# Optimization experiments

Measured on AMD Instinct MI355X. Metric: run time of the kernel, lower is better.

## Reference

```python
import jax, jax.numpy as jnp
from jax import lax
import numpy as np

LRELU = 0.01

def conv(x, w, b=None, stride=1, pad=0):
    y = lax.conv_general_dilated(x, w, (stride, stride), [(pad, pad), (pad, pad)],
                                 dimension_numbers=('NCHW', 'OIHW', 'NCHW'))
    return y if b is None else y + b[None, :, None, None]

def deconv(x, w, b, stride=2, pad=1):
    # torch ConvTranspose2d (w: [Cin, Cout, k, k]) == lhs-dilated conv with flipped kernel
    k = w.shape[2]
    wf = jnp.transpose(jnp.flip(w, (2, 3)), (1, 0, 2, 3))  # -> OIHW
    y = lax.conv_general_dilated(x, wf, (1, 1), [(k - 1 - pad, k - 1 - pad)] * 2,
                                 lhs_dilation=(stride, stride),
                                 dimension_numbers=('NCHW', 'OIHW', 'NCHW'))
    return y + b[None, :, None, None]

def bn(x, g, b, eps=1e-5):
    # training-mode BatchNorm2d: batch statistics over (N, H, W)
    m = x.mean((0, 2, 3), keepdims=True)
    v = x.var((0, 2, 3), keepdims=True)
    return (x - m) * lax.rsqrt(v + eps) * g[None, :, None, None] + b[None, :, None, None]

def resblock(x, w1, g1, b1, w2, g2, b2):
    h = jax.nn.relu(bn(conv(x, w1, pad=1), g1, b1))
    return x + bn(conv(h, w2), g2, b2)

def vq_quantize(z, emb, beta=0.25):
    zt = jnp.transpose(z, (0, 2, 3, 1))              # [B,H,W,D]
    D = zt.shape[-1]
    flat = zt.reshape(-1, D)                         # [M,D]
    dist = ((flat ** 2).sum(1, keepdims=True) + (emb ** 2).sum(1)
            - 2.0 * flat @ emb.T)                    # [M,K]
    idx = jnp.argmin(dist, axis=1)                   # [M]
    q = emb[idx].reshape(zt.shape)                   # gather == one-hot @ emb
    loss = beta * jnp.mean((lax.stop_gradient(q) - zt) ** 2)
    q_st = zt + lax.stop_gradient(q - zt)            # straight-through estimator
    counts = jnp.zeros((emb.shape[0],), flat.dtype).at[idx].add(1.0)
    probs = counts / flat.shape[0]
    perplexity = jnp.exp(-jnp.sum(probs * jnp.log(probs + 1e-10)))
    return jnp.transpose(q_st, (0, 3, 1, 2)), loss, perplexity

def vqvae_forward(p, x):
    h = jax.nn.leaky_relu(conv(x, p['e1w'], p['e1b'], 2, 1), LRELU)
    h = jax.nn.leaky_relu(conv(h, p['e2w'], p['e2b'], 2, 1), LRELU)
    h = jax.nn.leaky_relu(conv(h, p['e3w'], p['e3b'], 1, 1), LRELU)
    h = resblock(h, p['er1w'], p['er1g'], p['er1b'], p['er2w'], p['er2g'], p['er2b'])
    h = jax.nn.leaky_relu(h, LRELU)
    encoded = jax.nn.leaky_relu(conv(h, p['e4w'], p['e4b']), LRELU)
    quantized, vq_loss, _ = vq_quantize(encoded, p['emb'])
    h = jax.nn.leaky_relu(conv(quantized, p['d1w'], p['d1b'], 1, 1), LRELU)
    h = resblock(h, p['dr1w'], p['dr1g'], p['dr1b'], p['dr2w'], p['dr2g'], p['dr2b'])
    h = jax.nn.leaky_relu(h, LRELU)
    h = jax.nn.leaky_relu(deconv(h, p['dt1w'], p['dt1b']), LRELU)
    recon = jnp.tanh(deconv(h, p['dt2w'], p['dt2b']))
    return recon, quantized, encoded, vq_loss

def setup_inputs():
    key = jax.random.key(0)
    ks = iter(jax.random.split(key, 40))
    def w(shape, s=0.05):
        return jax.random.normal(next(ks), shape, jnp.float32) * s
    D, K = 64, 512
    return {
        'x': jax.random.normal(next(ks), (64, 3, 128, 128), jnp.float32),
        'e1w': w((32, 3, 4, 4)), 'e1b': jnp.zeros((32,), jnp.float32),
        'e2w': w((64, 32, 4, 4)), 'e2b': jnp.zeros((64,), jnp.float32),
        'e3w': w((64, 64, 3, 3)), 'e3b': jnp.zeros((64,), jnp.float32),
        'er1w': w((64, 64, 3, 3)), 'er1g': jnp.ones((64,), jnp.float32), 'er1b': jnp.zeros((64,), jnp.float32),
        'er2w': w((64, 64, 1, 1)), 'er2g': jnp.ones((64,), jnp.float32), 'er2b': jnp.zeros((64,), jnp.float32),
        'e4w': w((D, 64, 1, 1)), 'e4b': jnp.zeros((D,), jnp.float32),
        'emb': jax.random.normal(next(ks), (K, D), jnp.float32),
        'd1w': w((64, D, 3, 3)), 'd1b': jnp.zeros((64,), jnp.float32),
        'dr1w': w((64, 64, 3, 3)), 'dr1g': jnp.ones((64,), jnp.float32), 'dr1b': jnp.zeros((64,), jnp.float32),
        'dr2w': w((64, 64, 1, 1)), 'dr2g': jnp.ones((64,), jnp.float32), 'dr2b': jnp.zeros((64,), jnp.float32),
        'dt1w': w((64, 32, 4, 4)), 'dt1b': jnp.zeros((32,), jnp.float32),
        'dt2w': w((32, 3, 4, 4)), 'dt2b': jnp.zeros((3,), jnp.float32),
    }

def reference(x, e1w, e1b, e2w, e2b, e3w, e3b, er1w, er1g, er1b, er2w, er2g, er2b,
              e4w, e4b, emb, d1w, d1b, dr1w, dr1g, dr1b, dr2w, dr2g, dr2b,
              dt1w, dt1b, dt2w, dt2b):
    p = dict(e1w=e1w, e1b=e1b, e2w=e2w, e2b=e2b, e3w=e3w, e3b=e3b,
             er1w=er1w, er1g=er1g, er1b=er1b, er2w=er2w, er2g=er2g, er2b=er2b,
             e4w=e4w, e4b=e4b, emb=emb, d1w=d1w, d1b=d1b,
             dr1w=dr1w, dr1g=dr1g, dr1b=dr1b, dr2w=dr2w, dr2g=dr2g, dr2b=dr2b,
             dt1w=dt1w, dt1b=dt1b, dt2w=dt2w, dt2b=dt2b)
    return vqvae_forward(p, x)
```

## Files before the change

### kernel.cpp

```cpp
#include <hip/hip_runtime.h>
#include <math.h>

#define LREL 0.01f
__device__ __forceinline__ float lrelu(float x) { return x > 0.f ? x : LREL * x; }
__device__ __forceinline__ float fast_tanh(float x) {
    x = fminf(fmaxf(x, -10.f), 10.f);
    float a = __expf(2.f * x);
    return (a - 1.f) / (a + 1.f);
}
__device__ __forceinline__ unsigned short f2bf(float f) {
    unsigned u = __float_as_uint(f);
    unsigned r = u + 0x7FFFu + ((u >> 16) & 1u);
    return (unsigned short)(r >> 16);
}
__device__ __forceinline__ float bf2f(unsigned short h) {
    return __uint_as_float(((unsigned)h) << 16);
}

typedef __attribute__((ext_vector_type(8))) short short8;
typedef __attribute__((ext_vector_type(4))) float f32x4;

__global__ void __launch_bounds__(256) conv_e1_t(
    const float* __restrict__ x, const float* __restrict__ w,
    const float* __restrict__ bias,
    unsigned short* __restrict__ outH, unsigned short* __restrict__ outL)
{
    __shared__ float lin[3][18][131];
    __shared__ float lw[3][16][16];
    int b = blockIdx.x;
    int n = b & 63, t = b >> 6;
    int rt = t & 7, cg = t >> 3;
    int tid = threadIdx.x;
    int r = tid >> 5, g = tid & 31;
    const float* inp = x + (size_t)n * 3 * 16384;

    #pragma unroll
    for (int ci = 0; ci < 3; ++ci)
        if (tid < 36) lin[ci][tid >> 1][(tid & 1) ? 129 : 0] = 0.f;
    #pragma unroll
    for (int ci = 0; ci < 3; ++ci)
        #pragma unroll
        for (int k = 0; k < 9; ++k) {
            int idx = k * 256 + tid;
            int row = idx >> 7, col = idx & 127;
            int gy = 16 * rt - 1 + row;
            float v = 0.f;
            if (gy >= 0 && gy < 128)
                v = inp[ci * 16384 + gy * 128 + col];
            lin[ci][row][col + 1] = v;
        }
    for (int i = tid; i < 768; i += 256) {
        int ci = i >> 8, rr = i & 255, co = rr >> 4, tt = rr & 15;
        lw[ci][co][tt] = w[((cg * 16 + co) * 3 + ci) * 16 + tt];
    }
    __syncthreads();

    float acc[16][2];
    #pragma unroll
    for (int co = 0; co < 16; ++co) { acc[co][0] = acc[co][1] = 0.f; }

    #pragma unroll
    for (int ci = 0; ci < 3; ++ci) {
        float win[4][6];
        #pragma unroll
        for (int ky = 0; ky < 4; ++ky)
            #pragma unroll
            for (int dx = 0; dx < 6; ++dx)
                win[ky][dx] = lin[ci][2 * r + ky][4 * g + dx];
        #pragma unroll
        for (int co = 0; co < 16; ++co) {
            #pragma unroll
            for (int ky = 0; ky < 4; ++ky)
                #pragma unroll
                for (int kx = 0; kx < 4; ++kx) {
                    float wv = lw[ci][co][ky * 4 + kx];
                    acc[co][0] = fmaf(win[ky][kx],     wv, acc[co][0]);
                    acc[co][1] = fmaf(win[ky][kx + 2], wv, acc[co][1]);
                }
        }
    }
    int oy = 8 * rt + r;
    size_t base0 = (((size_t)n * 4096 + oy * 64 + 2 * g) * 32 + cg * 16);
    unsigned h0[8], l0[8], h1[8], l1[8];
    #pragma unroll
    for (int p = 0; p < 8; ++p) {
        float bva = bias[cg * 16 + 2 * p];
        float bvb = bias[cg * 16 + 2 * p + 1];
        float va0 = lrelu(acc[2 * p][0] + bva),     vb0 = lrelu(acc[2 * p + 1][0] + bvb);
        float va1 = lrelu(acc[2 * p][1] + bva),     vb1 = lrelu(acc[2 * p + 1][1] + bvb);
        unsigned short ha0 = f2bf(va0), hb0 = f2bf(vb0);
        unsigned short ha1 = f2bf(va1), hb1 = f2bf(vb1);
        h0[p] = (unsigned)ha0 | ((unsigned)hb0 << 16);
        h1[p] = (unsigned)ha1 | ((unsigned)hb1 << 16);
        l0[p] = (unsigned)f2bf(va0 - bf2f(ha0)) | ((unsigned)f2bf(vb0 - bf2f(hb0)) << 16);
        l1[p] = (unsigned)f2bf(va1 - bf2f(ha1)) | ((unsigned)f2bf(vb1 - bf2f(hb1)) << 16);
    }
    unsigned* oH0 = (unsigned*)(outH + base0);
    unsigned* oL0 = (unsigned*)(outL + base0);
    unsigned* oH1 = (unsigned*)(outH + base0 + 32);
    unsigned* oL1 = (unsigned*)(outL + base0 + 32);
    #pragma unroll
    for (int p = 0; p < 8; ++p) {
        oH0[p] = h0[p]; oL0[p] = l0[p];
        oH1[p] = h1[p]; oL1[p] = l1[p];
    }
}

__global__ void __launch_bounds__(256) mfma_e2_k(
    const unsigned short* __restrict__ inH, const unsigned short* __restrict__ inL,
    const float* __restrict__ w, const float* __restrict__ bias,
    unsigned short* __restrict__ outH, unsigned short* __restrict__ outL)
{
    __shared__ unsigned short linH[11][66][8], linL[11][66][8];
    __shared__ unsigned short lwH[64][152], lwL[64][152];
    int b = blockIdx.x;
    int n = b >> 3, ryt = b & 7;
    int tid = threadIdx.x;
    int wv = tid >> 6, l = tid & 63;
    int l15 = l & 15, lhi = l >> 4;

    f32x4 acc[4][2];
    #pragma unroll
    for (int ct = 0; ct < 4; ++ct)
        #pragma unroll
        for (int pt = 0; pt < 2; ++pt) {
            f32x4 z = {0.f, 0.f, 0.f, 0.f};
            acc[ct][pt] = z;
        }

    for (int cc = 0; cc < 4; ++cc) {
        __syncthreads();
        for (int i = tid; i < 726; i += 256) {
            int row = i / 66, col = i % 66;
            int gy = 8 * ryt - 1 + row, gx = col - 1;
            uint4 vH = make_uint4(0u, 0u, 0u, 0u);
            uint4 vL = make_uint4(0u, 0u, 0u, 0u);
            if (gy >= 0 && gy < 64 && gx >= 0 && gx < 64) {
                size_t gi = (((size_t)n * 4096 + gy * 64 + gx) * 32 + cc * 8);
                vH = *(const uint4*)(inH + gi);
                vL = *(const uint4*)(inL + gi);
            }
            *(uint4*)&linH[row][col][0] = vH;
            *(uint4*)&linL[row][col][0] = vL;
        }
        for (int i = tid; i < 8192; i += 256) {
            int co = i >> 7, rr = i & 127;
            int ky = rr >> 5, kx = (rr >> 3) & 3, j = rr & 7;
            float wv0 = w[(co * 32 + cc * 8 + j) * 16 + ky * 4 + kx];
            unsigned short h = f2bf(wv0);
            lwH[co][ky * 32 + kx * 8 + j] = h;
            lwL[co][ky * 32 + kx * 8 + j] = f2bf(wv0 - bf2f(h));
        }
        __syncthreads();

        #pragma unroll
        for (int kg = 0; kg < 4; ++kg) {
            short8 bH[2], bL[2];
            #pragma unroll
            for (int pt = 0; pt < 2; ++pt) {
                int col = 2 * (pt * 16 + l15) + lhi;
                bH[pt] = *(const short8*)&linH[2 * wv + kg][col][0];
                bL[pt] = *(const short8*)&linL[2 * wv + kg][col][0];
            }
            #pragma unroll
            for (int ct = 0; ct < 4; ++ct) {
                short8 aH = *(const short8*)&lwH[ct * 16 + l15][kg * 32 + lhi * 8];
                short8 aL = *(const short8*)&lwL[ct * 16 + l15][kg * 32 + lhi * 8];
                #pragma unroll
                for (int pt = 0; pt < 2; ++pt) {
                    acc[ct][pt] = __builtin_amdgcn_mfma_f32_16x16x32_bf16(aH, bH[pt], acc[ct][pt], 0, 0, 0);
                    acc[ct][pt] = __builtin_amdgcn_mfma_f32_16x16x32_bf16(aH, bL[pt], acc[ct][pt], 0, 0, 0);
                    acc[ct][pt] = __builtin_amdgcn_mfma_f32_16x16x32_bf16(aL, bH[pt], acc[ct][pt], 0, 0, 0);
                }
            }
        }
    }

    int oy = 4 * ryt + wv;
    #pragma unroll
    for (int pt = 0; pt < 2; ++pt) {
        int ox = pt * 16 + l15;
        size_t base = (((size_t)n * 1024 + oy * 32 + ox) << 6);
        #pragma unroll
        for (int ct = 0; ct < 4; ++ct) {
            int co0 = ct * 16 + lhi * 4;
            #pragma unroll
            for (int jp = 0; jp < 2; ++jp) {
                float v0 = lrelu(acc[ct][pt][2 * jp]     + bias[co0 + 2 * jp]);
                float v1 = lrelu(acc[ct][pt][2 * jp + 1] + bias[co0 + 2 * jp + 1]);
                unsigned short h0 = f2bf(v0), h1 = f2bf(v1);
                *(unsigned*)(outH + base + co0 + 2 * jp) = (unsigned)h0 | ((unsigned)h1 << 16);
                *(unsigned*)(outL + base + co0 + 2 * jp) =
                    (unsigned)f2bf(v0 - bf2f(h0)) | ((unsigned)f2bf(v1 - bf2f(h1)) << 16);
            }
        }
    }
}

template<int IN, int ACT, int STATS>
__global__ void __launch_bounds__(256) conv1x1_t(
    const float* __restrict__ in, const float* __restrict__ res,
    const float* __restrict__ w, const float* __restrict__ bias,
    const float* __restrict__ fin, const float* __restrict__ g,
    const float* __restrict__ beta, float* __restrict__ out,
    float* __restrict__ psum, float* __restrict__ pss)
{
    __shared__ float lw[64][64];
    __shared__ float sga[64], sbb[64];
    int b = blockIdx.x;
    int n = b >> 3, pxb = b & 7;
    int tid = threadIdx.x;
    int pxg = tid & 31, cog = tid >> 5;
    for (int i = tid; i < 4096; i += 256) {
        int co = i >> 6, ci = i & 63;
        lw[ci][co] = w[co * 64 + ci];
    }
    if (IN >= 1 && tid < 64) {
        float ga = g[tid] * fin[2 * tid + 1];
        sga[tid] = ga;
        sbb[tid] = beta[tid] - fin[2 * tid] * ga;
    }
    __syncthreads();

    size_t base = (size_t)n * 65536 + pxb * 128 + pxg * 4;
    float acc[8][4];
    #pragma unroll
    for (int co = 0; co < 8; ++co) { acc[co][0]=acc[co][1]=acc[co][2]=acc[co][3]=0.f; }
    #pragma unroll 4
    for (int ci = 0; ci < 64; ++ci) {
        float4 xv = *(const float4*)(in + base + (size_t)ci * 1024);
        float x0, x1, x2, x3;
        if (IN == 1) {
            float ga = sga[ci], bb = sbb[ci];
            x0 = fmaxf(fmaf(xv.x, ga, bb), 0.f);
            x1 = fmaxf(fmaf(xv.y, ga, bb), 0.f);
            x2 = fmaxf(fmaf(xv.z, ga, bb), 0.f);
            x3 = fmaxf(fmaf(xv.w, ga, bb), 0.f);
        } else if (IN == 2) {
            float4 rv = *(const float4*)(res + base + (size_t)ci * 1024);
            float ga = sga[ci], bb = sbb[ci];
            x0 = lrelu(rv.x + fmaf(xv.x, ga, bb));
            x1 = lrelu(rv.y + fmaf(xv.y, ga, bb));
            x2 = lrelu(rv.z + fmaf(xv.z, ga, bb));
            x3 = lrelu(rv.w + fmaf(xv.w, ga, bb));
        } else {
            x0 = xv.x; x1 = xv.y; x2 = xv.z; x3 = xv.w;
        }
        const float4* wr = (const float4*)&lw[ci][cog * 8];
        float4 wa = wr[0], wb = wr[1];
        acc[0][0] = fmaf(x0, wa.x, acc[0][0]); acc[0][1] = fmaf(x1, wa.x, acc[0][1]);
        acc[0][2] = fmaf(x2, wa.x, acc[0][2]); acc[0][3] = fmaf(x3, wa.x, acc[0][3]);
        acc[1][0] = fmaf(x0, wa.y, acc[1][0]); acc[1][1] = fmaf(x1, wa.y, acc[1][1]);
        acc[1][2] = fmaf(x2, wa.y, acc[1][2]); acc[1][3] = fmaf(x3, wa.y, acc[1][3]);
        acc[2][0] = fmaf(x0, wa.z, acc[2][0]); acc[2][1] = fmaf(x1, wa.z, acc[2][1]);
        acc[2][2] = fmaf(x2, wa.z, acc[2][2]); acc[2][3] = fmaf(x3, wa.z, acc[2][3]);
        acc[3][0] = fmaf(x0, wa.w, acc[3][0]); acc[3][1] = fmaf(x1, wa.w, acc[3][1]);
        acc[3][2] = fmaf(x2, wa.w, acc[3][2]); acc[3][3] = fmaf(x3, wa.w, acc[3][3]);
        acc[4][0] = fmaf(x0, wb.x, acc[4][0]); acc[4][1] = fmaf(x1, wb.x, acc[4][1]);
        acc[4][2] = fmaf(x2, wb.x, acc[4][2]); acc[4][3] = fmaf(x3, wb.x, acc[4][3]);
        acc[5][0] = fmaf(x0, wb.y, acc[5][0]); acc[5][1] = fmaf(x1, wb.y, acc[5][1]);
        acc[5][2] = fmaf(x2, wb.y, acc[5][2]); acc[5][3] = fmaf(x3, wb.y, acc[5][3]);
        acc[6][0] = fmaf(x0, wb.z, acc[6][0]); acc[6][1] = fmaf(x1, wb.z, acc[6][1]);
        acc[6][2] = fmaf(x2, wb.z, acc[6][2]); acc[6][3] = fmaf(x3, wb.z, acc[6][3]);
        acc[7][0] = fmaf(x0, wb.w, acc[7][0]); acc[7][1] = fmaf(x1, wb.w, acc[7][1]);
        acc[7][2] = fmaf(x2, wb.w, acc[7][2]); acc[7][3] = fmaf(x3, wb.w, acc[7][3]);
    }
    #pragma unroll
    for (int co = 0; co < 8; ++co) {
        int coG = cog * 8 + co;
        float bv = bias ? bias[coG] : 0.f;
        float a0 = acc[co][0] + bv, a1 = acc[co][1] + bv, a2 = acc[co][2] + bv, a3 = acc[co][3] + bv;
        if (ACT == 1) { a0 = lrelu(a0); a1 = lrelu(a1); a2 = lrelu(a2); a3 = lrelu(a3); }
        float4 v; v.x = a0; v.y = a1; v.z = a2; v.w = a3;
        *(float4*)(out + base + (size_t)coG * 1024) = v;
        if (STATS) {
            float s = a0 + a1 + a2 + a3;
            float q = a0*a0 + a1*a1 + a2*a2 + a3*a3;
            #pragma unroll
            for (int m = 1; m < 32; m <<= 1) {
                s += __shfl_xor(s, m);
                q += __shfl_xor(q, m);
            }
            if (pxg == 0) {
                psum[(size_t)coG * 512 + n * 8 + pxb] = s;
                pss [(size_t)coG * 512 + n * 8 + pxb] = q;
            }
        }
    }
}

__global__ void bn_fin2_k(const float* __restrict__ psum, const float* __restrict__ pss,
                          float* __restrict__ fin, float invM, int cnt)
{
    __shared__ float s1[64][4], s2[64][4];
    int c = threadIdx.x >> 2, part = threadIdx.x & 3;
    int per = cnt >> 2;
    float s = 0.f, q = 0.f;
    for (int i = part * per; i < (part + 1) * per; ++i) {
        s += psum[(size_t)c * cnt + i];
        q += pss[(size_t)c * cnt + i];
    }
    s1[c][part] = s; s2[c][part] = q;
    __syncthreads();
    if (part == 0) {
        float ss = s1[c][0] + s1[c][1] + s1[c][2] + s1[c][3];
        float qq = s2[c][0] + s2[c][1] + s2[c][2] + s2[c][3];
        float mean = ss * invM;
        float var  = qq * invM - mean * mean;
        fin[2 * c] = mean;
        fin[2 * c + 1] = rsqrtf(var + 1e-5f);
    }
}

__global__ void bn_fin3_k(const float* __restrict__ psum, const float* __restrict__ pss,
                          float* __restrict__ fin, float invM)
{
    int c = threadIdx.x;
    if (c >= 64) return;
    float s = 0.f, q = 0.f;
    for (int i = 0; i < 256; ++i) { s += psum[c * 256 + i]; q += pss[c * 256 + i]; }
    float mean = s * invM;
    float var  = q * invM - mean * mean;
    fin[2 * c] = mean;
    fin[2 * c + 1] = rsqrtf(var + 1e-5f);
}

template<int MODE>
__global__ void __launch_bounds__(256) trans_k(
    const float* __restrict__ in, const float* __restrict__ fin,
    const float* __restrict__ g, const float* __restrict__ beta,
    unsigned short* __restrict__ outT)
{
    __shared__ unsigned short tt[256][68];
    __shared__ float sga[64], sbb[64];
    int b = blockIdx.x;
    int n = b >> 2, pxb = b & 3;
    int tid = threadIdx.x;
    if (MODE == 1) {
        if (tid < 64) {
            float ga = g[tid] * fin[2 * tid + 1];
            sga[tid] = ga;
            sbb[tid] = beta[tid] - fin[2 * tid] * ga;
        }
        __syncthreads();
    }
    for (int i = tid; i < 16384; i += 256) {
        int ci = i >> 8, px = i & 255;
        float v = in[((size_t)(n * 64 + ci) << 10) + pxb * 256 + px];
        if (MODE == 1) v = fmaxf(fmaf(v, sga[ci], sbb[ci]), 0.f);
        tt[px][ci] = f2bf(v);
    }
    __syncthreads();
    for (int o = tid; o < 4096; o += 256) {
        int px = o >> 4, c4 = o & 15;
        uint2 v = *(const uint2*)&tt[px][c4 * 4];
        *(uint2*)(outT + ((((size_t)n << 10) + pxb * 256 + px) << 6) + c4 * 4) = v;
    }
}

template<int INM>
__global__ void __launch_bounds__(256) trans_hl_k(
    const float* __restrict__ inA, const float* __restrict__ inB,
    const float* __restrict__ bias2,
    unsigned short* __restrict__ outH, unsigned short* __restrict__ outL)
{
    __shared__ unsigned short th[256][68];
    __shared__ unsigned short tl[256][68];
    __shared__ float sb[64];
    int b = blockIdx.x;
    int n = b >> 2, pxb = b & 3;
    int tid = threadIdx.x;
    if (INM == 1 && tid < 64) sb[tid] = bias2[tid];
    if (INM == 1) __syncthreads();
    for (int i = tid; i < 16384; i += 256) {
        int ci = i >> 8, px = i & 255;
        size_t gi = ((size_t)(n * 64 + ci) << 10) + pxb * 256 + px;
        float v = inA[gi];
        if (INM == 1) v = lrelu(v + inB[gi] + sb[ci]);
        unsigned short h = f2bf(v);
        th[px][ci] = h;
        tl[px][ci] = f2bf(v - bf2f(h));
    }
    __syncthreads();
    for (int o = tid; o < 4096; o += 256) {
        int px = o >> 4, c4 = o & 15;
        size_t oidx = ((((size_t)n << 10) + pxb * 256 + px) << 6) + c4 * 4;
        *(uint2*)(outH + oidx) = *(const uint2*)&th[px][c4 * 4];
        *(uint2*)(outL + oidx) = *(const uint2*)&tl[px][c4 * 4];
    }
}

__global__ void __launch_bounds__(256) bnres_trans_k(
    const float* __restrict__ xin, const float* __restrict__ res,
    const float* __restrict__ fin, const float* __restrict__ g,
    const float* __restrict__ beta, unsigned short* __restrict__ outT)
{
    __shared__ unsigned short tt[256][68];
    __shared__ float sga[64], sbb[64];
    int b = blockIdx.x;
    int n = b >> 2, pxb = b & 3;
    int tid = threadIdx.x;
    if (tid < 64) {
        float ga = g[tid] * fin[2 * tid + 1];
        sga[tid] = ga;
        sbb[tid] = beta[tid] - fin[2 * tid] * ga;
    }
    __syncthreads();
    for (int i = tid; i < 16384; i += 256) {
        int ci = i >> 8, px = i & 255;
        size_t gi = ((size_t)(n * 64 + ci) << 10) + pxb * 256 + px;
        float v = lrelu(res[gi] + fmaf(xin[gi], sga[ci], sbb[ci]));
        tt[px][ci] = f2bf(v);
    }
    __syncthreads();
    for (int o = tid; o < 4096; o += 256) {
        int px = o >> 4, c4 = o & 15;
        uint2 v = *(const uint2*)&tt[px][c4 * 4];
        *(uint2*)(outT + ((((size_t)n << 10) + pxb * 256 + px) << 6) + c4 * 4) = v;
    }
}

template<int ACT, int STATS>
__global__ void __launch_bounds__(256) mfma_conv3x3_k(
    const unsigned short* __restrict__ inT, const float* __restrict__ w,
    const float* __restrict__ bias, float* __restrict__ out,
    float* __restrict__ psum, float* __restrict__ pss)
{
    __shared__ unsigned short lin[10][34][40];
    __shared__ unsigned short lwA[32][296];
    __shared__ float sS[4][32], sQ[4][32];
    int b = blockIdx.x;
    int cg = b & 1, pxb = (b >> 1) & 3, n = b >> 3;
    int tid = threadIdx.x;
    int wv = tid >> 6, l = tid & 63;
    int l15 = l & 15, lhi = l >> 4;

    f32x4 acc[2][4];
    #pragma unroll
    for (int ct = 0; ct < 2; ++ct)
        #pragma unroll
        for (int bt = 0; bt < 4; ++bt) {
            f32x4 z = {0.f, 0.f, 0.f, 0.f};
            acc[ct][bt] = z;
        }

    for (int c2 = 0; c2 < 2; ++c2) {
        __syncthreads();
        for (int i = tid; i < 1360; i += 256) {
            int pos = i >> 2, q = i & 3;
            int row = pos / 34, col = pos % 34;
            int iy = pxb * 8 - 1 + row, ix = col - 1;
            uint4 v = make_uint4(0u, 0u, 0u, 0u);
            if (iy >= 0 && iy < 32 && ix >= 0 && ix < 32)
                v = *(const uint4*)(inT + ((((size_t)n << 10) + iy * 32 + ix) << 6) + c2 * 32 + q * 8);
            *(uint4*)&lin[row][col][q * 8] = v;
        }
        for (int i = tid; i < 9216; i += 256) {
            int col = i / 288, k = i % 288;
            int tap = k >> 5, cc = k & 31;
            int co = cg * 32 + col;
            lwA[col][k] = f2bf(w[(co * 64 + c2 * 32 + cc) * 9 + tap]);
        }
        __syncthreads();
        #pragma unroll
        for (int tap = 0; tap < 9; ++tap) {
            const int dy = tap / 3, dx = tap % 3;
            short8 a[2], bb[4];
            #pragma unroll
            for (int ct = 0; ct < 2; ++ct)
                a[ct] = *(const short8*)&lwA[ct * 16 + l15][tap * 32 + lhi * 8];
            #pragma unroll
            for (int bt = 0; bt < 4; ++bt) {
                int rr = 2 * wv + (bt >> 1);
                int cc0 = (bt & 1) * 16;
                bb[bt] = *(const short8*)&lin[rr + dy][cc0 + l15 + dx][lhi * 8];
            }
            #pragma unroll
            for (int ct = 0; ct < 2; ++ct)
                #pragma unroll
                for (int bt = 0; bt < 4; ++bt)
                    acc[ct][bt] = __builtin_amdgcn_mfma_f32_16x16x32_bf16(a[ct], bb[bt], acc[ct][bt], 0, 0, 0);
        }
    }

    int orow0 = pxb * 8 + 2 * wv;
    #pragma unroll
    for (int ct = 0; ct < 2; ++ct) {
        #pragma unroll
        for (int j = 0; j < 4; ++j) {
            int co_l = ct * 16 + lhi * 4 + j;
            int co = cg * 32 + co_l;
            float bv = bias ? bias[co] : 0.f;
            float s = 0.f, q = 0.f;
            #pragma unroll
            for (int bt = 0; bt < 4; ++bt) {
                float v = acc[ct][bt][j] + bv;
                if (ACT == 1) v = lrelu(v);
                int row = orow0 + (bt >> 1);
                int col = (bt & 1) * 16 + l15;
                out[(((size_t)n * 64 + co) << 10) + row * 32 + col] = v;
                if (STATS) { s += v; q = fmaf(v, v, q); }
            }
            if (STATS) {
                #pragma unroll
                for (int m = 1; m < 16; m <<= 1) {
                    s += __shfl_xor(s, m);
                    q += __shfl_xor(q, m);
                }
                if (l15 == 0) { sS[wv][co_l] = s; sQ[wv][co_l] = q; }
            }
        }
    }
    if (STATS) {
        __syncthreads();
        if (tid < 32) {
            float s = sS[0][tid] + sS[1][tid] + sS[2][tid] + sS[3][tid];
            float q = sQ[0][tid] + sQ[1][tid] + sQ[2][tid] + sQ[3][tid];
            psum[(cg * 32 + tid) * 256 + n * 4 + pxb] = s;
            pss [(cg * 32 + tid) * 256 + n * 4 + pxb] = q;
        }
    }
}

template<int ACT, int STATS>
__global__ void __launch_bounds__(256) mfma_conv3x3_hl_k(
    const unsigned short* __restrict__ inH, const unsigned short* __restrict__ inL,
    const float* __restrict__ w, const float* __restrict__ bias,
    float* __restrict__ out, float* __restrict__ psum, float* __restrict__ pss)
{
    __shared__ unsigned short linH[10][34][40];
    __shared__ unsigned short linL[10][34][40];
    __shared__ unsigned short lwH[32][296];
    __shared__ unsigned short lwL[32][296];
    __shared__ float sS[4][32], sQ[4][32];
    int b = blockIdx.x;
    int cg = b & 1, pxb = (b >> 1) & 3, n = b >> 3;
    int tid = threadIdx.x;
    int wv = tid >> 6, l = tid & 63;
    int l15 = l & 15, lhi = l >> 4;

    f32x4 acc[2][4];
    #pragma unroll
    for (int ct = 0; ct < 2; ++ct)
        #pragma unroll
        for (int bt = 0; bt < 4; ++bt) {
            f32x4 z = {0.f, 0.f, 0.f, 0.f};
            acc[ct][bt] = z;
        }

    for (int c2 = 0; c2 < 2; ++c2) {
        __syncthreads();
        for (int i = tid; i < 1360; i += 256) {
            int pos = i >> 2, q = i & 3;
            int row = pos / 34, col = pos % 34;
            int iy = pxb * 8 - 1 + row, ix = col - 1;
            uint4 vh = make_uint4(0u, 0u, 0u, 0u);
            uint4 vl = make_uint4(0u, 0u, 0u, 0u);
            if (iy >= 0 && iy < 32 && ix >= 0 && ix < 32) {
                size_t gi = ((((size_t)n << 10) + iy * 32 + ix) << 6) + c2 * 32 + q * 8;
                vh = *(const uint4*)(inH + gi);
                vl = *(const uint4*)(inL + gi);
            }
            *(uint4*)&linH[row][col][q * 8] = vh;
            *(uint4*)&linL[row][col][q * 8] = vl;
        }
        for (int i = tid; i < 9216; i += 256) {
            int col = i / 288, k = i % 288;
            int tap = k >> 5, cc = k & 31;
            int co = cg * 32 + col;
            float wv0 = w[(co * 64 + c2 * 32 + cc) * 9 + tap];
            unsigned short h = f2bf(wv0);
            lwH[col][k] = h;
            lwL[col][k] = f2bf(wv0 - bf2f(h));
        }
        __syncthreads();
        #pragma unroll
        for (int tap = 0; tap < 9; ++tap) {
            const int dy = tap / 3, dx = tap % 3;
            short8 aH[2], aL[2], bH[4], bL[4];
            #pragma unroll
            for (int ct = 0; ct < 2; ++ct) {
                aH[ct] = *(const short8*)&lwH[ct * 16 + l15][tap * 32 + lhi * 8];
                aL[ct] = *(const short8*)&lwL[ct * 16 + l15][tap * 32 + lhi * 8];
            }
            #pragma unroll
            for (int bt = 0; bt < 4; ++bt) {
                int rr = 2 * wv + (bt >> 1);
                int cc0 = (bt & 1) * 16;
                bH[bt] = *(const short8*)&linH[rr + dy][cc0 + l15 + dx][lhi * 8];
                bL[bt] = *(const short8*)&linL[rr + dy][cc0 + l15 + dx][lhi * 8];
            }
            #pragma unroll
            for (int ct = 0; ct < 2; ++ct)
                #pragma unroll
                for (int bt = 0; bt < 4; ++bt) {
                    acc[ct][bt] = __builtin_amdgcn_mfma_f32_16x16x32_bf16(aH[ct], bH[bt], acc[ct][bt], 0, 0, 0);
                    acc[ct][bt] = __builtin_amdgcn_mfma_f32_16x16x32_bf16(aH[ct], bL[bt], acc[ct][bt], 0, 0, 0);
                    acc[ct][bt] = __builtin_amdgcn_mfma_f32_16x16x32_bf16(aL[ct], bH[bt], acc[ct][bt], 0, 0, 0);
                }
        }
    }

    int orow0 = pxb * 8 + 2 * wv;
    #pragma unroll
    for (int ct = 0; ct < 2; ++ct) {
        #pragma unroll
        for (int j = 0; j < 4; ++j) {
            int co_l = ct * 16 + lhi * 4 + j;
            int co = cg * 32 + co_l;
            float bv = bias ? bias[co] : 0.f;
            float s = 0.f, q = 0.f;
            #pragma unroll
            for (int bt = 0; bt < 4; ++bt) {
                float v = acc[ct][bt][j] + bv;
                if (ACT == 1) v = lrelu(v);
                int row = orow0 + (bt >> 1);
                int col = (bt & 1) * 16 + l15;
                out[(((size_t)n * 64 + co) << 10) + row * 32 + col] = v;
                if (STATS) { s += v; q = fmaf(v, v, q); }
            }
            if (STATS) {
                #pragma unroll
                for (int m = 1; m < 16; m <<= 1) {
                    s += __shfl_xor(s, m);
                    q += __shfl_xor(q, m);
                }
                if (l15 == 0) { sS[wv][co_l] = s; sQ[wv][co_l] = q; }
            }
        }
    }
    if (STATS) {
        __syncthreads();
        if (tid < 32) {
            float s = sS[0][tid] + sS[1][tid] + sS[2][tid] + sS[3][tid];
            float q = sQ[0][tid] + sQ[1][tid] + sQ[2][tid] + sQ[3][tid];
            psum[(cg * 32 + tid) * 256 + n * 4 + pxb] = s;
            pss [(cg * 32 + tid) * 256 + n * 4 + pxb] = q;
        }
    }
}

template<int ACT, int STATS>
__global__ void __launch_bounds__(256) mfma_conv1x1_k(
    const unsigned short* __restrict__ inT, const float* __restrict__ w,
    const float* __restrict__ bias, float* __restrict__ out,
    float* __restrict__ psum, float* __restrict__ pss)
{
    __shared__ unsigned short lin[256][72];
    __shared__ unsigned short lwA[32][72];
    __shared__ float sS[4][32], sQ[4][32];
    int b = blockIdx.x;
    int cg = b & 1, pxb = (b >> 1) & 3, n = b >> 3;
    int tid = threadIdx.x;
    int wv = tid >> 6, l = tid & 63;
    int l15 = l & 15, lhi = l >> 4;

    for (int i = tid; i < 2048; i += 256) {
        int px = i >> 3, q = i & 7;
        uint4 v = *(const uint4*)(inT + ((((size_t)n << 10) + pxb * 256 + px) << 6) + q * 8);
        *(uint4*)&lin[px][q * 8] = v;
    }
    for (int i = tid; i < 2048; i += 256) {
        int col = i >> 6, ci = i & 63;
        lwA[col][ci] = f2bf(w[(cg * 32 + col) * 64 + ci]);
    }
    __syncthreads();

    f32x4 acc[2][4];
    #pragma unroll
    for (int ct = 0; ct < 2; ++ct)
        #pragma unroll
        for (int bt = 0; bt < 4; ++bt) {
            f32x4 z = {0.f, 0.f, 0.f, 0.f};
            acc[ct][bt] = z;
        }

    #pragma unroll
    for (int ks = 0; ks < 2; ++ks) {
        short8 a[2], bb[4];
        #pragma unroll
        for (int ct = 0; ct < 2; ++ct)
            a[ct] = *(const short8*)&lwA[ct * 16 + l15][ks * 32 + lhi * 8];
        #pragma unroll
        for (int bt = 0; bt < 4; ++bt)
            bb[bt] = *(const short8*)&lin[wv * 64 + bt * 16 + l15][ks * 32 + lhi * 8];
        #pragma unroll
        for (int ct = 0; ct < 2; ++ct)
            #pragma unroll
            for (int bt = 0; bt < 4; ++bt)
                acc[ct][bt] = __builtin_amdgcn_mfma_f32_16x16x32_bf16(a[ct], bb[bt], acc[ct][bt], 0, 0, 0);
    }

    #pragma unroll
    for (int ct = 0; ct < 2; ++ct) {
        #pragma unroll
        for (int j = 0; j < 4; ++j) {
            int co_l = ct * 16 + lhi * 4 + j;
            int co = cg * 32 + co_l;
            float bv = bias ? bias[co] : 0.f;
            float s = 0.f, q = 0.f;
            #pragma unroll
            for (int bt = 0; bt < 4; ++bt) {
                float v = acc[ct][bt][j] + bv;
                if (ACT == 1) v = lrelu(v);
                int px = pxb * 256 + wv * 64 + bt * 16 + l15;
                out[(((size_t)n * 64 + co) << 10) + px] = v;
                if (STATS) { s += v; q = fmaf(v, v, q); }
            }
            if (STATS) {
                #pragma unroll
                for (int m = 1; m < 16; m <<= 1) {
                    s += __shfl_xor(s, m);
                    q += __shfl_xor(q, m);
                }
                if (l15 == 0) { sS[wv][co_l] = s; sQ[wv][co_l] = q; }
            }
        }
    }
    if (STATS) {
        __syncthreads();
        if (tid < 32) {
            float s = sS[0][tid] + sS[1][tid] + sS[2][tid] + sS[3][tid];
            float q = sQ[0][tid] + sQ[1][tid] + sQ[2][tid] + sQ[3][tid];
            psum[(cg * 32 + tid) * 256 + n * 4 + pxb] = s;
            pss [(cg * 32 + tid) * 256 + n * 4 + pxb] = q;
        }
    }
}

__global__ void __launch_bounds__(256) mfma_dt1_k(
    const unsigned short* __restrict__ inT, const float* __restrict__ w,
    const float* __restrict__ bias, float* __restrict__ out)
{
    __shared__ unsigned short lin[5][34][40];
    __shared__ unsigned short lwA[2][32][136];
    int b = blockIdx.x;
    int ublk = b & 7, p_y = (b >> 3) & 1, n = b >> 4;
    int tid = threadIdx.x;
    int wv = tid >> 6, l = tid & 63;
    int l15 = l & 15, lhi = l >> 4;
    int pq = wv & 1;
    int vbase = 1 - pq;
    int ubase = ublk * 4 + (p_y == 0 ? 1 : 0);

    f32x4 acc[2][4];
    #pragma unroll
    for (int ct = 0; ct < 2; ++ct)
        #pragma unroll
        for (int bt = 0; bt < 4; ++bt) {
            f32x4 z = {0.f, 0.f, 0.f, 0.f};
            acc[ct][bt] = z;
        }

    for (int ch = 0; ch < 2; ++ch) {
        __syncthreads();
        for (int i = tid; i < 680; i += 256) {
            int rr = i / 136, rem = i % 136;
            int jc = rem >> 2, q = rem & 3;
            int gy = ubase - 1 + rr, gx = jc - 1;
            uint4 v = make_uint4(0u, 0u, 0u, 0u);
            if (gy >= 0 && gy < 32 && gx >= 0 && gx < 32)
                v = *(const uint4*)(inT + ((((size_t)n << 10) + gy * 32 + gx) << 6) + ch * 32 + q * 8);
            *(uint4*)&lin[rr][jc][q * 8] = v;
        }
        for (int i = tid; i < 8192; i += 256) {
            int pqq = i >> 12, co = (i >> 7) & 31, k = i & 127;
            int tap = k >> 5, cc = k & 31;
            int ci = ch * 32 + cc;
            int ky = p_y + 2 * (tap >> 1), kx = pqq + 2 * (tap & 1);
            lwA[pqq][co][k] = f2bf(w[((ci * 32 + co) << 4) + ky * 4 + kx]);
        }
        __syncthreads();
        #pragma unroll
        for (int ks = 0; ks < 4; ++ks) {
            int ty = ks >> 1, tx = ks & 1;
            short8 a[2], bb[4];
            #pragma unroll
            for (int ct = 0; ct < 2; ++ct)
                a[ct] = *(const short8*)&lwA[pq][ct * 16 + l15][ks * 32 + lhi * 8];
            #pragma unroll
            for (int bt = 0; bt < 4; ++bt) {
                int jloc = (wv >> 1) * 2 + (bt >> 1);
                int vloc = (bt & 1) * 16 + l15;
                bb[bt] = *(const short8*)&lin[jloc + 1 - ty][vloc + vbase + 1 - tx][lhi * 8];
            }
            #pragma unroll
            for (int ct = 0; ct < 2; ++ct)
                #pragma unroll
                for (int bt = 0; bt < 4; ++bt)
                    acc[ct][bt] = __builtin_amdgcn_mfma_f32_16x16x32_bf16(a[ct], bb[bt], acc[ct][bt], 0, 0, 0);
        }
    }

    #pragma unroll
    for (int ct = 0; ct < 2; ++ct) {
        #pragma unroll
        for (int j = 0; j < 4; ++j) {
            int co = ct * 16 + lhi * 4 + j;
            float bv = bias[co];
            #pragma unroll
            for (int bt = 0; bt < 4; ++bt) {
                int jloc = (wv >> 1) * 2 + (bt >> 1);
                int vloc = (bt & 1) * 16 + l15;
                int oy = 2 * (ubase + jloc) - 1 + p_y;
                int ox = 2 * (vloc + vbase) - 1 + pq;
                out[((size_t)(n * 32 + co) << 12) + oy * 64 + ox] = lrelu(acc[ct][bt][j] + bv);
            }
        }
    }
}

__device__ __forceinline__ unsigned order_u32(float s) {
    unsigned u = __float_as_uint(s);
    return (s < 0.f) ? ~u : (u | 0x80000000u);
}
__device__ __forceinline__ unsigned long long min_u64(unsigned long long a, unsigned long long b) {
    return a < b ? a : b;
}

__global__ void __launch_bounds__(256) vq_dist_mfma_k(
    const float* __restrict__ z, const float* __restrict__ emb,
    unsigned long long* __restrict__ best)
{
    __shared__ unsigned short zH[128][72], zL[128][72];
    __shared__ unsigned short eH[128][72], eL[128][72];
    __shared__ float en[128];
    int b = blockIdx.x;
    int n = b >> 3, pxb = b & 7;
    int tid = threadIdx.x;
    int wv = tid >> 6, l = tid & 63;
    int l15 = l & 15, lhi = l >> 4;

    #pragma unroll
    for (int k = 0; k < 32; ++k) {
        int idx = k * 256 + tid;
        int d = idx >> 7, px = idx & 127;
        float v = z[(size_t)n * 65536 + (size_t)d * 1024 + pxb * 128 + px];
        unsigned short h = f2bf(v);
        zH[px][d] = h;
        zL[px][d] = f2bf(v - bf2f(h));
    }

    unsigned long long bb0 = ~0ULL, bb1 = ~0ULL;

    for (int ch = 0; ch < 4; ++ch) {
        __syncthreads();
        if (ch > 0) __syncthreads();
        #pragma unroll
        for (int k = 0; k < 32; ++k) {
            int idx = k * 256 + tid;
            int kc = idx >> 6, d = idx & 63;
            float v = emb[(size_t)(ch * 128 + kc) * 64 + d];
            unsigned short h = f2bf(v);
            eH[kc][d] = h;
            eL[kc][d] = f2bf(v - bf2f(h));
        }
        if (tid < 128) {
            const float4* e4 = (const float4*)(emb + (size_t)(ch * 128 + tid) * 64);
            float s = 0.f;
            #pragma unroll
            for (int j = 0; j < 16; ++j) {
                float4 e = e4[j];
                s = fmaf(e.x, e.x, s); s = fmaf(e.y, e.y, s);
                s = fmaf(e.z, e.z, s); s = fmaf(e.w, e.w, s);
            }
            en[tid] = s;
        }
        __syncthreads();

        #pragma unroll
        for (int pt = 0; pt < 2; ++pt) {
            int px = (wv * 2 + pt) * 16 + l15;
            short8 zh0 = *(const short8*)&zH[px][lhi * 8];
            short8 zh1 = *(const short8*)&zH[px][32 + lhi * 8];
            short8 zl0 = *(const short8*)&zL[px][lhi * 8];
            short8 zl1 = *(const short8*)&zL[px][32 + lhi * 8];
            unsigned long long bbl = (pt == 0) ? bb0 : bb1;
            #pragma unroll
            for (int ct2 = 0; ct2 < 8; ++ct2) {
                f32x4 acc = {0.f, 0.f, 0.f, 0.f};
                short8 eh0 = *(const short8*)&eH[ct2 * 16 + l15][lhi * 8];
                short8 eh1 = *(const short8*)&eH[ct2 * 16 + l15][32 + lhi * 8];
                short8 el0 = *(const short8*)&eL[ct2 * 16 + l15][lhi * 8];
                short8 el1 = *(const short8*)&eL[ct2 * 16 + l15][32 + lhi * 8];
                acc = __builtin_amdgcn_mfma_f32_16x16x32_bf16(eh0, zh0, acc, 0, 0, 0);
                acc = __builtin_amdgcn_mfma_f32_16x16x32_bf16(eh1, zh1, acc, 0, 0, 0);
                acc = __builtin_amdgcn_mfma_f32_16x16x32_bf16(eh0, zl0, acc, 0, 0, 0);
                acc = __builtin_amdgcn_mfma_f32_16x16x32_bf16(eh1, zl1, acc, 0, 0, 0);
                acc = __builtin_amdgcn_mfma_f32_16x16x32_bf16(el0, zh0, acc, 0, 0, 0);
                acc = __builtin_amdgcn_mfma_f32_16x16x32_bf16(el1, zh1, acc, 0, 0, 0);
                int kb = ch * 128 + ct2 * 16 + lhi * 4;
                #pragma unroll
                for (int j = 0; j < 4; ++j) {
                    float dist = fmaf(-2.f, acc[j], en[ct2 * 16 + lhi * 4 + j]);
                    unsigned long long p = ((unsigned long long)order_u32(dist) << 32) | (unsigned)(kb + j);
                    bbl = min_u64(bbl, p);
                }
            }
            if (pt == 0) bb0 = bbl; else bb1 = bbl;
        }
    }

    #pragma unroll
    for (int pt = 0; pt < 2; ++pt) {
        unsigned long long v = (pt == 0) ? bb0 : bb1;
        v = min_u64(v, __shfl_xor(v, 16));
        v = min_u64(v, __shfl_xor(v, 32));
        if (lhi == 0) {
            int px = (wv * 2 + pt) * 16 + l15;
            best[(size_t)n * 1024 + pxb * 128 + px] = v;
        }
    }
}

__global__ void __launch_bounds__(256) vq_combine_k(
    const float* __restrict__ z, const float* __restrict__ emb,
    const unsigned long long* __restrict__ best,
    float* __restrict__ out_q, unsigned short* __restrict__ outT,
    float* __restrict__ partials)
{
    __shared__ unsigned tq32[256][33];
    __shared__ float sh[256];
    int tid = threadIdx.x;
    int m = blockIdx.x * 256 + tid;
    unsigned long long bb = best[m];
    int bi = (int)(bb & 0x1ffu);
    int n = m >> 10, p = m & 1023;
    size_t base = (size_t)n * 65536 + p;
    const float* eb = emb + (bi << 6);
    float lsum = 0.f;
    #pragma unroll
    for (int d = 0; d < 64; d += 2) {
        float z0 = z[base + (size_t)d * 1024];
        float z1 = z[base + (size_t)(d + 1) * 1024];
        float q0 = eb[d], q1 = eb[d + 1];
        out_q[base + (size_t)d * 1024]       = q0;
        out_q[base + (size_t)(d + 1) * 1024] = q1;
        float d0 = q0 - z0, d1 = q1 - z1;
        lsum = fmaf(d0, d0, lsum);
        lsum = fmaf(d1, d1, lsum);
        tq32[tid][d >> 1] = (unsigned)f2bf(q0) | ((unsigned)f2bf(q1) << 16);
    }
    sh[tid] = lsum;
    __syncthreads();
    unsigned* oT = (unsigned*)outT;
    size_t m0 = (size_t)blockIdx.x * 256;
    #pragma unroll
    for (int k = 0; k < 32; ++k) {
        int j = k * 256 + tid;
        int px = j >> 5, c = j & 31;
        oT[(m0 + px) * 32 + c] = tq32[px][c];
    }
    for (int st = 128; st > 0; st >>= 1) {
        if (tid < st) sh[tid] += sh[tid + st];
        __syncthreads();
    }
    if (tid == 0) partials[blockIdx.x] = sh[0];
}

__global__ void vq_fin_k(const float* __restrict__ partials, float* __restrict__ out)
{
    __shared__ float sh[256];
    sh[threadIdx.x] = partials[threadIdx.x];
    __syncthreads();
    for (int st = 128; st > 0; st >>= 1) {
        if (threadIdx.x < st) sh[threadIdx.x] += sh[threadIdx.x + st];
        __syncthreads();
    }
    if (threadIdx.x == 0) out[0] = sh[0] * (0.25f / (65536.f * 64.f));
}

__global__ void __launch_bounds__(256) deconv_dt2_t(
    const float* __restrict__ in, const float* __restrict__ w,
    const float* __restrict__ bias, float* __restrict__ out)
{
    __shared__ float lin[8][4][67];
    __shared__ float lw[8][3][16];
    int b = blockIdx.x;
    int n = b & 63, rt = b >> 6;
    int tid = threadIdx.x;
    int r4 = tid >> 6, g = tid & 63;
    int oy = rt * 4 + r4;
    const float* inp = in + (size_t)n * 32 * 4096;
    int iy0 = 2 * rt - 1;
    int ky0 = (oy + 1) & 1;
    int iyA = ((oy + 1 - ky0) >> 1) - iy0;
    int iyB = iyA - 1;

    if (tid < 64) lin[tid >> 3][(tid >> 1) & 3][(tid & 1) ? 65 : 0] = 0.f;

    float acc[3][2];
    #pragma unroll
    for (int co = 0; co < 3; ++co) { acc[co][0] = acc[co][1] = 0.f; }

    int scol = tid & 63, srs = tid >> 6;
    for (int cic = 0; cic < 4; ++cic) {
        __syncthreads();
        {
            int gy = iy0 + srs;
            bool ok = (gy >= 0 && gy < 64);
            #pragma unroll
            for (int k = 0; k < 8; ++k) {
                float v = ok ? inp[(cic * 8 + k) * 4096 + gy * 64 + scol] : 0.f;
                lin[k][srs][scol + 1] = v;
            }
        }
        if (tid < 128) {
            int ci = tid >> 4, tt = tid & 15;
            #pragma unroll
            for (int co = 0; co < 3; ++co)
                lw[ci][co][tt] = w[((cic * 8 + ci) * 3 + co) * 16 + tt];
        }
        __syncthreads();
        #pragma unroll 2
        for (int ci = 0; ci < 8; ++ci) {
            float vA0 = lin[ci][iyA][g],     vA1 = lin[ci][iyA][g + 1], vA2 = lin[ci][iyA][g + 2];
            float vB0 = lin[ci][iyB][g],     vB1 = lin[ci][iyB][g + 1], vB2 = lin[ci][iyB][g + 2];
            #pragma unroll
            for (int co = 0; co < 3; ++co) {
                const float4* wp = (const float4*)lw[ci][co];
                float4 wA = wp[ky0];
                float4 wB = wp[ky0 + 2];
                acc[co][0] = fmaf(vA1, wA.y, fmaf(vA0, wA.w, fmaf(vB1, wB.y, fmaf(vB0, wB.w, acc[co][0]))));
                acc[co][1] = fmaf(vA2, wA.x, fmaf(vA1, wA.z, fmaf(vB2, wB.x, fmaf(vB1, wB.z, acc[co][1]))));
            }
        }
    }
    #pragma unroll
    for (int co = 0; co < 3; ++co) {
        float bv = bias[co];
        float2 v;
        v.x = fast_tanh(acc[co][0] + bv);
        v.y = fast_tanh(acc[co][1] + bv);
        *(float2*)(out + ((size_t)(n * 3 + co) * 16384) + oy * 128 + 2 * g) = v;
    }
}

extern "C" void kernel_launch(void* const* d_in, const int* in_sizes, int n_in,
                              void* d_out, int out_size, void* d_ws, size_t ws_size,
                              hipStream_t stream)
{
    const float* x    = (const float*)d_in[0];
    const float* e1w  = (const float*)d_in[1];
    const float* e1b  = (const float*)d_in[2];
    const float* e2w  = (const float*)d_in[3];
    const float* e2b  = (const float*)d_in[4];
    const float* e3w  = (const float*)d_in[5];
    const float* e3b  = (const float*)d_in[6];
    const float* er1w = (const float*)d_in[7];
    const float* er1g = (const float*)d_in[8];
    const float* er1b = (const float*)d_in[9];
    const float* er2w = (const float*)d_in[10];
    const float* er2g = (const float*)d_in[11];
    const float* er2b = (const float*)d_in[12];
    const float* e4w  = (const float*)d_in[13];
    const float* e4b  = (const float*)d_in[14];
    const float* emb  = (const float*)d_in[15];
    const float* d1w  = (const float*)d_in[16];
    const float* d1b  = (const float*)d_in[17];
    const float* dr1w = (const float*)d_in[18];
    const float* dr1g = (const float*)d_in[19];
    const float* dr1b = (const float*)d_in[20];
    const float* dr2w = (const float*)d_in[21];
    const float* dr2g = (const float*)d_in[22];
    const float* dr2b = (const float*)d_in[23];
    const float* dt1w = (const float*)d_in[24];
    const float* dt1b = (const float*)d_in[25];
    const float* dt2w = (const float*)d_in[26];
    const float* dt2b = (const float*)d_in[27];

    float* out = (float*)d_out;
    float* ws  = (float*)d_ws;

    float* B0 = ws;
    float* B1 = ws + 8388608;
    float* B2 = B1 + 4194304;
    float* B3 = B2 + 4194304;
    float* B4 = B3 + 4194304;
    float* psum   = B4 + 4194304;
    float* pss    = psum + 32768;
    float* fin    = pss + 32768;
    float* vq_part = fin + 128;
    unsigned long long* bestbuf = (unsigned long long*)(vq_part + 256);

    unsigned short* e1H  = (unsigned short*)B0;
    unsigned short* e1L  = e1H + 8388608;
    unsigned short* tbuf  = (unsigned short*)B1;
    unsigned short* tbufH = (unsigned short*)B3;
    unsigned short* tbufL = (unsigned short*)B4;

    float* out_recon = out;
    float* out_q     = out + 3145728;
    float* out_e     = out + 7340032;
    float* out_loss  = out + 11534336;

    const float invM = 1.f / 65536.f;

    conv_e1_t<<<1024, 256, 0, stream>>>(x, e1w, e1b, e1H, e1L);
    mfma_e2_k<<<512, 256, 0, stream>>>(e1H, e1L, e2w, e2b, tbufH, tbufL);

    mfma_conv3x3_hl_k<1,0><<<512, 256, 0, stream>>>(tbufH, tbufL, e3w, e3b, B2, nullptr, nullptr);

    trans_hl_k<0><<<256, 256, 0, stream>>>(B2, nullptr, nullptr, tbufH, tbufL);
    mfma_conv3x3_hl_k<0,1><<<512, 256, 0, stream>>>(tbufH, tbufL, er1w, nullptr, B1, psum, pss);
    bn_fin3_k<<<1, 64, 0, stream>>>(psum, pss, fin, invM);

    conv1x1_t<1,0,1><<<512, 256, 0, stream>>>(B1, nullptr, er2w, nullptr, fin, er1g, er1b, B4, psum, pss);
    bn_fin2_k<<<1, 256, 0, stream>>>(psum, pss, fin, invM, 512);
    conv1x1_t<2,1,0><<<512, 256, 0, stream>>>(B4, B2, e4w, e4b, fin, er2g, er2b, out_e, nullptr, nullptr);

    vq_dist_mfma_k<<<512, 256, 0, stream>>>(out_e, emb, bestbuf);
    vq_combine_k<<<256, 256, 0, stream>>>(out_e, emb, bestbuf, out_q, tbuf, vq_part);
    vq_fin_k<<<1, 256, 0, stream>>>(vq_part, out_loss);

    mfma_conv3x3_k<1,0><<<512, 256, 0, stream>>>(tbuf, d1w, d1b, B2, nullptr, nullptr);

    trans_k<0><<<256, 256, 0, stream>>>(B2, nullptr, nullptr, nullptr, tbuf);
    mfma_conv3x3_k<0,1><<<512, 256, 0, stream>>>(tbuf, dr1w, nullptr, B3, psum, pss);
    bn_fin3_k<<<1, 64, 0, stream>>>(psum, pss, fin, invM);

    trans_k<1><<<256, 256, 0, stream>>>(B3, fin, dr1g, dr1b, tbuf);
    mfma_conv1x1_k<0,1><<<512, 256, 0, stream>>>(tbuf, dr2w, nullptr, B4, psum, pss);
    bn_fin3_k<<<1, 64, 0, stream>>>(psum, pss, fin, invM);

    bnres_trans_k<<<256, 256, 0, stream>>>(B4, B2, fin, dr2g, dr2b, tbuf);
    mfma_dt1_k<<<1024, 256, 0, stream>>>(tbuf, dt1w, dt1b, B0);

    deconv_dt2_t<<<2048, 256, 0, stream>>>(B0, dt2w, dt2b, out_recon);
}
```

Before: 503.6 us.

## Enlarge e2 MFMA conv tile with even/odd split LDS layout

```diff
diff --git a/kernel.cpp b/kernel.cpp
--- a/kernel.cpp
+++ b/kernel.cpp
@@ -111,28 +111,33 @@
     const float* __restrict__ w, const float* __restrict__ bias,
     unsigned short* __restrict__ outH, unsigned short* __restrict__ outL)
 {
-    __shared__ unsigned short linH[11][66][8], linL[11][66][8];
-    __shared__ unsigned short lwH[64][152], lwL[64][152];
+    __shared__ unsigned short lEH[18][34][8], lEL[18][34][8];
+    __shared__ unsigned short lOH[18][34][8], lOL[18][34][8];
+    __shared__ unsigned short lwH[64][136], lwL[64][136];
     int b = blockIdx.x;
-    int n = b >> 3, ryt = b & 7;
+    int n = b >> 2, rq = b & 3;
     int tid = threadIdx.x;
     int wv = tid >> 6, l = tid & 63;
     int l15 = l & 15, lhi = l >> 4;
 
-    f32x4 acc[4][2];
+    f32x4 acc[4][2][2];
     #pragma unroll
     for (int ct = 0; ct < 4; ++ct)
         #pragma unroll
-        for (int pt = 0; pt < 2; ++pt) {
-            f32x4 z = {0.f, 0.f, 0.f, 0.f};
-            acc[ct][pt] = z;
-        }
+        for (int rs = 0; rs < 2; ++rs)
+            #pragma unroll
+            for (int pt = 0; pt < 2; ++pt) {
+                f32x4 z = {0.f, 0.f, 0.f, 0.f};
+                acc[ct][rs][pt] = z;
+            }
 
     for (int cc = 0; cc < 4; ++cc) {
         __syncthreads();
-        for (int i = tid; i < 726; i += 256) {
-            int row = i / 66, col = i % 66;
-            int gy = 8 * ryt - 1 + row, gx = col - 1;
+        for (int i = tid; i < 1188; i += 256) {
+            int row = i / 66, rem = i % 66;
+            int par = rem & 1, cp = rem >> 1;
+            int gy = 16 * rq - 1 + row;
+            int gx = 2 * cp - 1 + par;
             uint4 vH = make_uint4(0u, 0u, 0u, 0u);
             uint4 vL = make_uint4(0u, 0u, 0u, 0u);
             if (gy >= 0 && gy < 64 && gx >= 0 && gx < 64) {
@@ -140,8 +145,13 @@
                 vH = *(const uint4*)(inH + gi);
                 vL = *(const uint4*)(inL + gi);
             }
-            *(uint4*)&linH[row][col][0] = vH;
-            *(uint4*)&linL[row][col][0] = vL;
+            if (par == 0) {
+                *(uint4*)&lEH[row][cp][0] = vH;
+                *(uint4*)&lEL[row][cp][0] = vL;
+            } else {
+                *(uint4*)&lOH[row][cp][0] = vH;
+                *(uint4*)&lOL[row][cp][0] = vL;
+            }
         }
         for (int i = tid; i < 8192; i += 256) {
             int co = i >> 7, rr = i & 127;
@@ -155,43 +165,58 @@
 
         #pragma unroll
         for (int kg = 0; kg < 4; ++kg) {
-            short8 bH[2], bL[2];
-            #pragma unroll
-            for (int pt = 0; pt < 2; ++pt) {
-                int col = 2 * (pt * 16 + l15) + lhi;
-                bH[pt] = *(const short8*)&linH[2 * wv + kg][col][0];
-                bL[pt] = *(const short8*)&linL[2 * wv + kg][col][0];
+            short8 bH[2][2], bL[2][2];
+            int cpo = lhi >> 1;
+            #pragma unroll
+            for (int rs = 0; rs < 2; ++rs) {
+                int row = 4 * wv + 2 * rs + kg;
+                #pragma unroll
+                for (int pt = 0; pt < 2; ++pt) {
+                    int cpp = pt * 16 + l15 + cpo;
+                    if (lhi & 1) {
+                        bH[rs][pt] = *(const short8*)&lOH[row][cpp][0];
+                        bL[rs][pt] = *(const short8*)&lOL[row][cpp][0];
+                    } else {
+                        bH[rs][pt] = *(const short8*)&lEH[row][cpp][0];
+                        bL[rs][pt] = *(const short8*)&lEL[row][cpp][0];
+                    }
+                }
             }
             #pragma unroll
             for (int ct = 0; ct < 4; ++ct) {
                 short8 aH = *(const short8*)&lwH[ct * 16 + l15][kg * 32 + lhi * 8];
                 short8 aL = *(const short8*)&lwL[ct * 16 + l15][kg * 32 + lhi * 8];
                 #pragma unroll
-                for (int pt = 0; pt < 2; ++pt) {
-                    acc[ct][pt] = __builtin_amdgcn_mfma_f32_16x16x32_bf16(aH, bH[pt], acc[ct][pt], 0, 0, 0);
-                    acc[ct][pt] = __builtin_amdgcn_mfma_f32_16x16x32_bf16(aH, bL[pt], acc[ct][pt], 0, 0, 0);
-                    acc[ct][pt] = __builtin_amdgcn_mfma_f32_16x16x32_bf16(aL, bH[pt], acc[ct][pt], 0, 0, 0);
+                for (int rs = 0; rs < 2; ++rs)
+                    #pragma unroll
+                    for (int pt = 0; pt < 2; ++pt) {
+                        acc[ct][rs][pt] = __builtin_amdgcn_mfma_f32_16x16x32_bf16(aH, bH[rs][pt], acc[ct][rs][pt], 0, 0, 0);
+                        acc[ct][rs][pt] = __builtin_amdgcn_mfma_f32_16x16x32_bf16(aH, bL[rs][pt], acc[ct][rs][pt], 0, 0, 0);
+                        acc[ct][rs][pt] = __builtin_amdgcn_mfma_f32_16x16x32_bf16(aL, bH[rs][pt], acc[ct][rs][pt], 0, 0, 0);
+                    }
+            }
+        }
+    }
+
+    #pragma unroll
+    for (int rs = 0; rs < 2; ++rs) {
+        int oy = 8 * rq + 2 * wv + rs;
+        #pragma unroll
+        for (int pt = 0; pt < 2; ++pt) {
+            int ox = pt * 16 + l15;
+            size_t base = (((size_t)n * 1024 + oy * 32 + ox) << 6);
+            #pragma unroll
+            for (int ct = 0; ct < 4; ++ct) {
+                int co0 = ct * 16 + lhi * 4;
+                #pragma unroll
+                for (int jp = 0; jp < 2; ++jp) {
+                    float v0 = lrelu(acc[ct][rs][pt][2 * jp]     + bias[co0 + 2 * jp]);
+                    float v1 = lrelu(acc[ct][rs][pt][2 * jp + 1] + bias[co0 + 2 * jp + 1]);
+                    unsigned short h0 = f2bf(v0), h1 = f2bf(v1);
+                    *(unsigned*)(outH + base + co0 + 2 * jp) = (unsigned)h0 | ((unsigned)h1 << 16);
+                    *(unsigned*)(outL + base + co0 + 2 * jp) =
+                        (unsigned)f2bf(v0 - bf2f(h0)) | ((unsigned)f2bf(v1 - bf2f(h1)) << 16);
                 }
-            }
-        }
-    }
-
-    int oy = 4 * ryt + wv;
-    #pragma unroll
-    for (int pt = 0; pt < 2; ++pt) {
-        int ox = pt * 16 + l15;
-        size_t base = (((size_t)n * 1024 + oy * 32 + ox) << 6);
-        #pragma unroll
-        for (int ct = 0; ct < 4; ++ct) {
-            int co0 = ct * 16 + lhi * 4;
-            #pragma unroll
-            for (int jp = 0; jp < 2; ++jp) {
-                float v0 = lrelu(acc[ct][pt][2 * jp]     + bias[co0 + 2 * jp]);
-                float v1 = lrelu(acc[ct][pt][2 * jp + 1] + bias[co0 + 2 * jp + 1]);
-                unsigned short h0 = f2bf(v0), h1 = f2bf(v1);
-                *(unsigned*)(outH + base + co0 + 2 * jp) = (unsigned)h0 | ((unsigned)h1 << 16);
-                *(unsigned*)(outL + base + co0 + 2 * jp) =
-                    (unsigned)f2bf(v0 - bf2f(h0)) | ((unsigned)f2bf(v1 - bf2f(h1)) << 16);
             }
         }
     }
@@ -845,7 +870,6 @@
 
     for (int ch = 0; ch < 4; ++ch) {
         __syncthreads();
-        if (ch > 0) __syncthreads();
         #pragma unroll
         for (int k = 0; k < 32; ++k) {
             int idx = k * 256 + tid;
@@ -1097,7 +1121,7 @@
     const float invM = 1.f / 65536.f;
 
     conv_e1_t<<<1024, 256, 0, stream>>>(x, e1w, e1b, e1H, e1L);
-    mfma_e2_k<<<512, 256, 0, stream>>>(e1H, e1L, e2w, e2b, tbufH, tbufL);
+    mfma_e2_k<<<256, 256, 0, stream>>>(e1H, e1L, e2w, e2b, tbufH, tbufL);
 
     mfma_conv3x3_hl_k<1,0><<<512, 256, 0, stream>>>(tbufH, tbufL, e3w, e3b, B2, nullptr, nullptr);
 
```

Result: no change. 497.1 us (-1.3%).
